# Performance work log

Hardware: AMD Instinct MI355X
Metric: run time of the kernel (lower is better)

The kernel has to match this reference:

```python
import jax, jax.numpy as jnp
import numpy as np

NUM_BLOCKS = 8
SPARSITY = 0.01
HARD_FRAC = 1.0
LN_EPS = 1e-5


def layer_norm(x, w, b):
    mu = jnp.mean(x, axis=-1, keepdims=True)
    var = jnp.mean(jnp.square(x - mu), axis=-1, keepdims=True)
    return (x - mu) * jax.lax.rsqrt(var + LN_EPS) * w + b


def softshrink(v, lam):
    return jnp.sign(v) * jnp.maximum(jnp.abs(v) - lam, 0.0)


def afno2d(x, w1, b1, w2, b2):
    # x: [B,H,W,C] float32
    bias = x
    B, H, W, C = x.shape
    nb = NUM_BLOCKS
    bs = C // nb
    xf = jnp.fft.rfft2(x, axes=(1, 2), norm='ortho')  # [B,H,W//2+1,C] complex
    Wf = W // 2 + 1
    xf = xf.reshape(B, H, Wf, nb, bs)
    total_modes = H // 2 + 1
    kept = int(total_modes * HARD_FRAC)
    lo = total_modes - kept
    hi = min(H, total_modes + kept)
    xs = xf[:, lo:hi, :kept]  # [B,hs,kept,nb,bs]
    xr, xi = xs.real, xs.imag
    o1r = jax.nn.relu(jnp.einsum('bhwki,kio->bhwko', xr, w1[0])
                      - jnp.einsum('bhwki,kio->bhwko', xi, w1[1]) + b1[0])
    o1i = jax.nn.relu(jnp.einsum('bhwki,kio->bhwko', xi, w1[0])
                      + jnp.einsum('bhwki,kio->bhwko', xr, w1[1]) + b1[1])
    o2r = (jnp.einsum('bhwko,koi->bhwki', o1r, w2[0])
           - jnp.einsum('bhwko,koi->bhwki', o1i, w2[1]) + b2[0])
    o2i = (jnp.einsum('bhwko,koi->bhwki', o1i, w2[0])
           + jnp.einsum('bhwko,koi->bhwki', o1r, w2[1]) + b2[1])
    o2r = softshrink(o2r, SPARSITY)
    o2i = softshrink(o2i, SPARSITY)
    oc = o2r + 1j * o2i
    full = jnp.zeros((B, H, Wf, nb, bs), dtype=oc.dtype)
    full = full.at[:, lo:hi, :kept].set(oc)
    full = full.reshape(B, H, Wf, C)
    out = jnp.fft.irfft2(full, s=(H, W), axes=(1, 2), norm='ortho')
    return out + bias


def setup_inputs() -> dict:
    key = jax.random.key(0)
    ks = jax.random.split(key, 12)
    B, H, W, C = 2, 90, 180, 768
    nb = NUM_BLOCKS
    bs = C // nb
    hidden = 4 * C
    scale = 0.02
    return {
        'x': jax.random.normal(ks[0], (B, H, W, C), jnp.float32),
        'norm1_w': jnp.ones((C,), jnp.float32),
        'norm1_b': jnp.zeros((C,), jnp.float32),
        'w1': scale * jax.random.normal(ks[1], (2, nb, bs, bs), jnp.float32),
        'b1': scale * jax.random.normal(ks[2], (2, nb, bs), jnp.float32),
        'w2': scale * jax.random.normal(ks[3], (2, nb, bs, bs), jnp.float32),
        'b2': scale * jax.random.normal(ks[4], (2, nb, bs), jnp.float32),
        'norm2_w': jnp.ones((C,), jnp.float32),
        'norm2_b': jnp.zeros((C,), jnp.float32),
        'fc1_w': jax.random.normal(ks[5], (C, hidden), jnp.float32) * (1.0 / np.sqrt(C)),
        'fc1_b': jnp.zeros((hidden,), jnp.float32),
        'fc2_w': jax.random.normal(ks[6], (hidden, C), jnp.float32) * (1.0 / np.sqrt(hidden)),
        'fc2_b': jnp.zeros((C,), jnp.float32),
    }


def reference(x, norm1_w, norm1_b, w1, b1, w2, b2, norm2_w, norm2_b,
              fc1_w, fc1_b, fc2_w, fc2_b):
    residual = x
    h = layer_norm(x, norm1_w, norm1_b)
    h = afno2d(h, w1, b1, w2, b2)
    # double_skip=True
    h = h + residual
    residual = h
    h = layer_norm(h, norm2_w, norm2_b)
    h = jax.nn.gelu(h @ fc1_w + fc1_b, approximate=False)
    h = h @ fc2_w + fc2_b
    return h + residual
```

## Files before the change

### kernel.cpp

```cpp
#include <hip/hip_runtime.h>
#include <hip/hip_bf16.h>

#define B_    2
#define H_    90
#define W_    180
#define C_    768
#define WFK   46
#define NBK   8
#define BSK   96
#define HID   3072
#define NTOK  (B_*H_*W_)
#define MPAD  32512
#define NPOS  (B_*H_*WFK)
#define LAM   0.01f

typedef __attribute__((ext_vector_type(8))) short short8;
typedef __attribute__((ext_vector_type(4))) float f32x4;

__device__ __forceinline__ float bf2f(short u) {
    union { unsigned int i; float f; } z;
    z.i = ((unsigned int)(unsigned short)u) << 16;
    return z.f;
}
__device__ __forceinline__ short f2b(float f) {
    return (short)__bfloat16_as_ushort(__float2bfloat16(f));
}

__device__ __forceinline__ void gload_lds16(const void* g, void* l) {
    __builtin_amdgcn_global_load_lds((const __attribute__((address_space(1))) void*)g,
                                     (__attribute__((address_space(3))) void*)l, 16, 0, 0);
}

__device__ __forceinline__ float gelu_f(float v) {
    float u = v * (0.7978845608028654f + 0.03567740813636141f * v * v);
    float au = fabsf(u);
    float e = __expf(2.f * au);
    float t = 1.f - 2.f / (e + 1.f);
    t = copysignf(t, u);
    return 0.5f * v * (1.f + t);
}

__global__ __launch_bounds__(256) void init_tables_kernel(__hip_bfloat16* Tw, __hip_bfloat16* Twf,
                                                          __hip_bfloat16* Thf, __hip_bfloat16* Thi) {
    int i = blockIdx.x * 256 + threadIdx.x;
    const float S = 0.00785674201318386f;
    if (i < 192 * 96) {
        int w = i / 96, k = i % 96;
        int j = k >> 1, odd = k & 1;
        float val = 0.f;
        if (w < W_ && j < WFK) {
            float th = (float)((w * j) % W_) * (float)(6.283185307179586476925286766559 / 180.0);
            if (odd) val = (j == 0) ? 0.f : -2.f * S * sinf(th);
            else     val = (j == 0) ? S : 2.f * S * cosf(th);
        }
        Tw[i] = __float2bfloat16(val);
    }
    if (i < 96 * 192) {
        int r = i / 192, w = i % 192;
        int wf = r >> 1, odd = r & 1;
        float val = 0.f;
        if (w < W_ && wf < WFK) {
            float th = (float)((w * wf) % W_) * (float)(6.283185307179586476925286766559 / 180.0);
            val = odd ? -S * sinf(th) : S * cosf(th);
        }
        Twf[i] = __float2bfloat16(val);
    }
    if (i < 192 * 192) {
        int r = i / 192, j = i % 192;
        float vf = 0.f, vi = 0.f;
        if (r < 180 && j < 180) {
            int k = r >> 1, ro = r & 1, h = j >> 1, jo = j & 1;
            float th = (float)((k * h) % H_) * (float)(6.283185307179586476925286766559 / 90.0);
            float c = cosf(th), s = sinf(th);
            vf = ro ? (jo ? c : -s) : (jo ? s : c);
            vi = ro ? (jo ? c : s) : (jo ? -s : c);
        }
        Thf[i] = __float2bfloat16(vf);
        Thi[i] = __float2bfloat16(vi);
    }
}

__global__ __launch_bounds__(256) void wprep_kernel(
        const float* __restrict__ w1, const float* __restrict__ b1,
        const float* __restrict__ w2, const float* __restrict__ b2,
        __hip_bfloat16* __restrict__ wbig, float* __restrict__ bbig)
{
    int idx = blockIdx.x * 256 + threadIdx.x;
    if (idx < 2 * NBK * 192 * 192) {
        int k = idx % 192;
        int o = (idx / 192) % 192;
        int nb = (idx / (192 * 192)) % NBK;
        int L = idx / (192 * 192 * NBK);
        const float* w = L ? w2 : w1;
        const float* wr = w + (size_t)nb * BSK * BSK;
        const float* wi = w + (size_t)(NBK + nb) * BSK * BSK;
        int kk = k % BSK, oo = o % BSK;
        float val;
        if (o < BSK)  val = (k < BSK) ? wr[kk * BSK + oo] : -wi[kk * BSK + oo];
        else          val = (k < BSK) ? wi[kk * BSK + oo] :  wr[kk * BSK + oo];
        wbig[((size_t)(L * NBK + nb) * 192 + o) * 192 + k] = __float2bfloat16(val);
    }
    if (idx < 2 * NBK * 192) {
        int o = idx % 192;
        int nb = (idx / 192) % NBK;
        int L = idx / (192 * NBK);
        const float* b = L ? b2 : b1;
        bbig[idx] = (o < BSK) ? b[nb * BSK + o] : b[(NBK + nb) * BSK + (o - BSK)];
    }
}

__global__ __launch_bounds__(256) void ln_kernel(const float* __restrict__ in,
        const float* __restrict__ w, const float* __restrict__ b,
        __hip_bfloat16* __restrict__ outb, int ntok_valid)
{
    int tok = blockIdx.x;
    int tid = threadIdx.x;
    size_t base = (size_t)tok * C_;
    if (tok >= ntok_valid) {
        __hip_bfloat16 z = __float2bfloat16(0.f);
        outb[base + tid] = z; outb[base + tid + 256] = z; outb[base + tid + 512] = z;
        return;
    }
    float x0 = in[base + tid], x1 = in[base + tid + 256], x2 = in[base + tid + 512];
    float s = x0 + x1 + x2;
    float q = x0*x0 + x1*x1 + x2*x2;
#pragma unroll
    for (int off = 32; off > 0; off >>= 1) { s += __shfl_down(s, off); q += __shfl_down(q, off); }
    __shared__ float rs[4], rq[4];
    int wid = tid >> 6, lane = tid & 63;
    if (lane == 0) { rs[wid] = s; rq[wid] = q; }
    __syncthreads();
    float ts = rs[0] + rs[1] + rs[2] + rs[3];
    float tq = rq[0] + rq[1] + rq[2] + rq[3];
    float mu = ts * (1.f / C_);
    float var = tq * (1.f / C_) - mu * mu;
    float rstd = rsqrtf(var + 1e-5f);
#pragma unroll
    for (int k = 0; k < 3; ++k) {
        int c = tid + k * 256;
        float xv = (k == 0 ? x0 : (k == 1 ? x1 : x2));
        outb[base + c] = __float2bfloat16((xv - mu) * rstd * w[c] + b[c]);
    }
}

__global__ __launch_bounds__(256) void wfft_kernel(const __hip_bfloat16* __restrict__ h1,
        short* __restrict__ f1r, short* __restrict__ f1i,
        const __hip_bfloat16* __restrict__ Twf)
{
    __shared__ __hip_bfloat16 Xt[64 * 200];
    int slab = blockIdx.x;
    int c0 = blockIdx.y * 64;
    int tid = threadIdx.x, wid = tid >> 6, lane = tid & 63;
    int lrow = lane & 15, lk8 = lane >> 4;
    const short* src = (const short*)h1 + (size_t)slab * W_ * C_ + c0;
    short* X = (short*)Xt;
    for (int i = tid; i < W_ * 8; i += 256) {
        int w = i >> 3, c8 = (i & 7) * 8;
        short8 v = *(const short8*)&src[(size_t)w * C_ + c8];
#pragma unroll
        for (int j = 0; j < 8; ++j) X[(c8 + j) * 200 + w] = v[j];
    }
    for (int z = tid; z < 64 * 12; z += 256) {
        int c = z / 12, w = 180 + z % 12;
        Xt[c * 200 + w] = __float2bfloat16(0.f);
    }
    __syncthreads();
    const short* Tp = (const short*)Twf;
    f32x4 zero = {0.f, 0.f, 0.f, 0.f};
    f32x4 acc[6];
#pragma unroll
    for (int m = 0; m < 6; ++m) acc[m] = zero;
#pragma unroll
    for (int ks = 0; ks < 6; ++ks) {
        short8 bf = *(const short8*)&X[(wid * 16 + lrow) * 200 + ks * 32 + lk8 * 8];
#pragma unroll
        for (int m = 0; m < 6; ++m) {
            short8 af = *(const short8*)&Tp[(m * 16 + lrow) * 192 + ks * 32 + lk8 * 8];
            acc[m] = __builtin_amdgcn_mfma_f32_16x16x32_bf16(af, bf, acc[m], 0, 0, 0);
        }
    }
    int crow = (lane >> 4) * 4, ccol = lane & 15;
#pragma unroll
    for (int m = 0; m < 6; ++m)
#pragma unroll
        for (int j = 0; j < 4; ++j) {
            int r = m * 16 + crow + j;
            int wf = r >> 1;
            if (wf >= WFK) continue;
            size_t o = ((size_t)slab * WFK + wf) * C_ + c0 + wid * 16 + ccol;
            if (r & 1) f1i[o] = f2b(acc[m][j]);
            else       f1r[o] = f2b(acc[m][j]);
        }
}

__global__ __launch_bounds__(256) void hdft_kernel(short* __restrict__ dr, short* __restrict__ di,
        const __hip_bfloat16* __restrict__ Th)
{
    __shared__ __hip_bfloat16 Xt[64 * 200];
    int bwf = blockIdx.x;
    int b = bwf / WFK, wf = bwf % WFK;
    int c0 = blockIdx.y * 64;
    int tid = threadIdx.x, wid = tid >> 6, lane = tid & 63;
    int lrow = lane & 15, lk8 = lane >> 4;
    size_t base = ((size_t)(b * H_) * WFK + wf) * C_ + c0;
    short* X = (short*)Xt;
    for (int i = tid; i < H_ * 8; i += 256) {
        int h = i >> 3, c8 = (i & 7) * 8;
        size_t a = base + (size_t)h * WFK * C_ + c8;
        short8 re = *(const short8*)&dr[a];
        short8 im = *(const short8*)&di[a];
#pragma unroll
        for (int j = 0; j < 8; ++j) {
            X[(c8 + j) * 200 + 2 * h]     = re[j];
            X[(c8 + j) * 200 + 2 * h + 1] = im[j];
        }
    }
    for (int z = tid; z < 64 * 12; z += 256) {
        int c = z / 12, j = 180 + z % 12;
        Xt[c * 200 + j] = __float2bfloat16(0.f);
    }
    __syncthreads();
    const short* Tp = (const short*)Th;
    f32x4 zero = {0.f, 0.f, 0.f, 0.f};
    f32x4 acc[3][4];
#pragma unroll
    for (int m = 0; m < 3; ++m)
#pragma unroll
        for (int n = 0; n < 4; ++n) acc[m][n] = zero;
#pragma unroll
    for (int ks = 0; ks < 6; ++ks) {
        short8 af[3], bf[4];
#pragma unroll
        for (int m = 0; m < 3; ++m)
            af[m] = *(const short8*)&Tp[(wid * 48 + m * 16 + lrow) * 192 + ks * 32 + lk8 * 8];
#pragma unroll
        for (int n = 0; n < 4; ++n)
            bf[n] = *(const short8*)&X[(n * 16 + lrow) * 200 + ks * 32 + lk8 * 8];
#pragma unroll
        for (int m = 0; m < 3; ++m)
#pragma unroll
            for (int n = 0; n < 4; ++n)
                acc[m][n] = __builtin_amdgcn_mfma_f32_16x16x32_bf16(af[m], bf[n], acc[m][n], 0, 0, 0);
    }
    int crow = (lane >> 4) * 4, ccol = lane & 15;
#pragma unroll
    for (int m = 0; m < 3; ++m)
#pragma unroll
        for (int j = 0; j < 4; ++j) {
            int r = wid * 48 + m * 16 + crow + j;
            int kh = r >> 1;
            if (kh >= H_) continue;
#pragma unroll
            for (int n = 0; n < 4; ++n) {
                size_t o = base + (size_t)kh * WFK * C_ + n * 16 + ccol;
                if (r & 1) di[o] = f2b(acc[m][n][j]);
                else       dr[o] = f2b(acc[m][n][j]);
            }
        }
}

__global__ __launch_bounds__(256) void blockmlp_mfma_kernel(
        short* __restrict__ vr, short* __restrict__ vi,
        const __hip_bfloat16* __restrict__ wbig, const float* __restrict__ bbig)
{
    __shared__ __hip_bfloat16 X1[64 * 200];
    __shared__ __hip_bfloat16 X2[64 * 200];
    int chunk = blockIdx.x;
    int nb = blockIdx.y;
    int tid = threadIdx.x, wid = tid >> 6, lane = tid & 63;
    int p0 = chunk * 64;
    short8 z8 = {0, 0, 0, 0, 0, 0, 0, 0};
    for (int i = tid; i < 64 * 24; i += 256) {
        int p = i / 24, q = i % 24;
        int pg = p0 + p;
        bool isr = q < 12;
        int c8 = (q % 12) * 8;
        short8 v = z8;
        if (pg < NPOS) {
            const short* src = isr ? vr : vi;
            v = *(const short8*)&src[(size_t)pg * C_ + nb * BSK + c8];
        }
        short* d = (short*)&X1[p * 200 + (isr ? 0 : 96) + c8];
#pragma unroll
        for (int j = 0; j < 8; ++j) d[j] = v[j];
    }
    __syncthreads();
    int n0 = wid * 48;
    int lrow = lane & 15, lk8 = lane >> 4;
    int crow = (lane >> 4) * 4, ccol = lane & 15;
    const short* W1 = (const short*)(wbig + (size_t)nb * 192 * 192);
    const short* W2 = (const short*)(wbig + (size_t)(NBK + nb) * 192 * 192);
    const float* bb1 = bbig + nb * 192;
    const float* bb2 = bbig + (NBK + nb) * 192;
    f32x4 zero = {0.f, 0.f, 0.f, 0.f};
    {
        f32x4 acc[4][3];
#pragma unroll
        for (int m = 0; m < 4; ++m)
#pragma unroll
            for (int n = 0; n < 3; ++n) acc[m][n] = zero;
#pragma unroll
        for (int k0 = 0; k0 < 192; k0 += 32) {
            short8 af[4], bf[3];
#pragma unroll
            for (int m = 0; m < 4; ++m)
                af[m] = *(const short8*)&X1[(m * 16 + lrow) * 200 + k0 + lk8 * 8];
#pragma unroll
            for (int n = 0; n < 3; ++n)
                bf[n] = *(const short8*)&W1[(size_t)(n0 + n * 16 + lrow) * 192 + k0 + lk8 * 8];
#pragma unroll
            for (int m = 0; m < 4; ++m)
#pragma unroll
                for (int n = 0; n < 3; ++n)
                    acc[m][n] = __builtin_amdgcn_mfma_f32_16x16x32_bf16(af[m], bf[n], acc[m][n], 0, 0, 0);
        }
        __syncthreads();
#pragma unroll
        for (int m = 0; m < 4; ++m)
#pragma unroll
            for (int j = 0; j < 4; ++j) {
                int row = m * 16 + crow + j;
#pragma unroll
                for (int n = 0; n < 3; ++n) {
                    int col = n0 + n * 16 + ccol;
                    float v = acc[m][n][j] + bb1[col];
                    X2[row * 200 + col] = __float2bfloat16(fmaxf(v, 0.f));
                }
            }
    }
    __syncthreads();
    {
        f32x4 acc[4][3];
#pragma unroll
        for (int m = 0; m < 4; ++m)
#pragma unroll
            for (int n = 0; n < 3; ++n) acc[m][n] = zero;
#pragma unroll
        for (int k0 = 0; k0 < 192; k0 += 32) {
            short8 af[4], bf[3];
#pragma unroll
            for (int m = 0; m < 4; ++m)
                af[m] = *(const short8*)&X2[(m * 16 + lrow) * 200 + k0 + lk8 * 8];
#pragma unroll
            for (int n = 0; n < 3; ++n)
                bf[n] = *(const short8*)&W2[(size_t)(n0 + n * 16 + lrow) * 192 + k0 + lk8 * 8];
#pragma unroll
            for (int m = 0; m < 4; ++m)
#pragma unroll
                for (int n = 0; n < 3; ++n)
                    acc[m][n] = __builtin_amdgcn_mfma_f32_16x16x32_bf16(af[m], bf[n], acc[m][n], 0, 0, 0);
        }
#pragma unroll
        for (int m = 0; m < 4; ++m)
#pragma unroll
            for (int j = 0; j < 4; ++j) {
                int row = m * 16 + crow + j;
                int pg = p0 + row;
                if (pg >= NPOS) continue;
#pragma unroll
                for (int n = 0; n < 3; ++n) {
                    int col = n0 + n * 16 + ccol;
                    float v = acc[m][n][j] + bb2[col];
                    v = v > LAM ? v - LAM : (v < -LAM ? v + LAM : 0.f);
                    if (col < BSK) vr[(size_t)pg * C_ + nb * BSK + col] = f2b(v);
                    else           vi[(size_t)pg * C_ + nb * BSK + col - BSK] = f2b(v);
                }
            }
    }
}

__global__ __launch_bounds__(256) void iwfft_kernel(
        const short* __restrict__ inr, const short* __restrict__ ini,
        const __hip_bfloat16* __restrict__ h1, const float* __restrict__ x,
        float* __restrict__ out, const __hip_bfloat16* __restrict__ Tw)
{
    __shared__ __hip_bfloat16 Yt[64 * 104];
    int slab = blockIdx.x;
    int c0 = blockIdx.y * 64;
    int tid = threadIdx.x, wid = tid >> 6, lane = tid & 63;
    int lrow = lane & 15, lk8 = lane >> 4;
    size_t sb = (size_t)slab * WFK * C_ + c0;
    short* Y = (short*)Yt;
    for (int i = tid; i < WFK * 8; i += 256) {
        int wf = i >> 3, c8 = (i & 7) * 8;
        size_t a = sb + (size_t)wf * C_ + c8;
        short8 re = *(const short8*)&inr[a];
        short8 im = *(const short8*)&ini[a];
#pragma unroll
        for (int j = 0; j < 8; ++j) {
            Y[(c8 + j) * 104 + 2 * wf]     = re[j];
            Y[(c8 + j) * 104 + 2 * wf + 1] = im[j];
        }
    }
    {
        int c = tid >> 2, kk = 92 + (tid & 3);
        Yt[c * 104 + kk] = __float2bfloat16(0.f);
    }
    __syncthreads();
    const short* Tp = (const short*)Tw;
    f32x4 zero = {0.f, 0.f, 0.f, 0.f};
    f32x4 acc[3][4];
#pragma unroll
    for (int m = 0; m < 3; ++m)
#pragma unroll
        for (int n = 0; n < 4; ++n) acc[m][n] = zero;
#pragma unroll
    for (int ks = 0; ks < 3; ++ks) {
        short8 af[3], bf[4];
#pragma unroll
        for (int m = 0; m < 3; ++m)
            af[m] = *(const short8*)&Tp[(wid * 48 + m * 16 + lrow) * 96 + ks * 32 + lk8 * 8];
#pragma unroll
        for (int n = 0; n < 4; ++n)
            bf[n] = *(const short8*)&Y[(n * 16 + lrow) * 104 + ks * 32 + lk8 * 8];
#pragma unroll
        for (int m = 0; m < 3; ++m)
#pragma unroll
            for (int n = 0; n < 4; ++n)
                acc[m][n] = __builtin_amdgcn_mfma_f32_16x16x32_bf16(af[m], bf[n], acc[m][n], 0, 0, 0);
    }
    int crow = (lane >> 4) * 4, ccol = lane & 15;
    const short* hp = (const short*)h1;
#pragma unroll
    for (int m = 0; m < 3; ++m)
#pragma unroll
        for (int j = 0; j < 4; ++j) {
            int w = wid * 48 + m * 16 + crow + j;
            if (w >= W_) continue;
            size_t o = ((size_t)slab * W_ + w) * C_ + c0;
#pragma unroll
            for (int n = 0; n < 4; ++n) {
                int col = n * 16 + ccol;
                out[o + col] = acc[m][n][j] + bf2f(hp[o + col]) + x[o + col];
            }
        }
}

__global__ __launch_bounds__(256) void transpose_cvt_kernel(const float* __restrict__ Wm,
        __hip_bfloat16* __restrict__ Wt, int R, int Ccol)
{
    __shared__ float tile[32][33];
    int c0 = blockIdx.x * 32, r0 = blockIdx.y * 32;
    int tid = threadIdx.x;
    int tc = tid & 31, tr = tid >> 5;
#pragma unroll
    for (int k = 0; k < 4; ++k)
        tile[tr + k * 8][tc] = Wm[(size_t)(r0 + tr + k * 8) * Ccol + c0 + tc];
    __syncthreads();
    int rr = tid & 31, cc = tid >> 5;
#pragma unroll
    for (int k = 0; k < 4; ++k)
        Wt[(size_t)(c0 + cc + k * 8) * R + r0 + rr] = __float2bfloat16(tile[rr][cc + k * 8]);
}

template<int EPI>
__global__ __launch_bounds__(512, 1) void gemm_kernel(
        const short* __restrict__ A, const short* __restrict__ Bt,
        const float* __restrict__ bias,
        __hip_bfloat16* __restrict__ obf, float* __restrict__ of32,
        const float* __restrict__ res, int N, int K, int mvalid, int MT, int NT)
{
    __shared__ short lds[73728];
    int nwg = MT * NT;
    int orig = blockIdx.x;
    int xcd = orig & 7, loc = orig >> 3;
    int q = nwg >> 3, rm = nwg & 7;
    int wg = (xcd < rm ? xcd * (q + 1) : rm * (q + 1) + (xcd - rm) * q) + loc;
    const int SUPER = 4;
    int per = SUPER * NT;
    int sidx = wg / per, offs = wg % per;
    int rows = MT - sidx * SUPER; if (rows > SUPER) rows = SUPER;
    int mt = sidx * SUPER + offs % rows;
    int nt = offs / rows;
    size_t m0 = (size_t)mt * 256, n0 = (size_t)nt * 128;

    int tid = threadIdx.x;
    int wid = tid >> 6, lane = tid & 63;
    int wmidx = wid >> 1, wnidx = wid & 1;
    int lrow = lane & 15, lk8 = lane >> 4;
    int rswz = (lk8 ^ ((lrow >> 1) & 3)) * 16;

    int sr = tid >> 2;
    int soct = (tid & 3) ^ ((sr >> 1) & 3);
    const short* Agbase = A + (m0 + sr) * (size_t)K + soct * 8;
    const short* Bgbase = Bt + (n0 + sr) * (size_t)K + soct * 8;
    int dA = sr * 64 + (tid & 3) * 16;
    f32x4 zero = {0.f, 0.f, 0.f, 0.f};
    f32x4 acc[4][4];
#pragma unroll
    for (int i = 0; i < 4; ++i)
#pragma unroll
        for (int j = 0; j < 4; ++j) acc[i][j] = zero;

    auto stage = [&](int buf, int kt) {
        const short* As0 = Agbase + kt * 64;
        const short* Bs0 = Bgbase + kt * 64;
        char* Ab = (char*)lds + buf * 49152 + dA;
        char* Bb = (char*)lds + buf * 49152 + 32768 + dA;
#pragma unroll
        for (int ksh = 0; ksh < 2; ++ksh) {
            gload_lds16(As0 + ksh * 32, Ab + ksh * 16384);
            gload_lds16(As0 + ksh * 32 + (size_t)128 * K, Ab + ksh * 16384 + 8192);
            gload_lds16(Bs0 + ksh * 32, Bb + ksh * 8192);
        }
    };

    int abase = (wmidx * 64 + lrow) * 64 + rswz;
    int bbase = 32768 + (wnidx * 64 + lrow) * 64 + rswz;

    int NK = K >> 6;
    stage(0, 0); stage(1, 1);
    for (int t = 0; t < NK; ++t) {
        int buf = t % 3;
        if (t + 2 < NK) stage((t + 2) % 3, t + 2);
        if (t + 2 < NK)      asm volatile("s_waitcnt vmcnt(12)" ::: "memory");
        else if (t + 1 < NK) asm volatile("s_waitcnt vmcnt(6)" ::: "memory");
        else                 asm volatile("s_waitcnt vmcnt(0)" ::: "memory");
        __builtin_amdgcn_sched_barrier(0);
        __builtin_amdgcn_s_barrier();
        __builtin_amdgcn_sched_barrier(0);
#pragma unroll
        for (int ks = 0; ks < 2; ++ks) {
            const char* L = (const char*)lds;
            short8 af[4], bfr[4];
            int ao = buf * 49152 + ks * 16384 + abase;
            int bo = buf * 49152 + ks * 8192 + bbase;
#pragma unroll
            for (int mf = 0; mf < 4; ++mf) af[mf] = *(const short8*)(L + ao + mf * 1024);
#pragma unroll
            for (int nf = 0; nf < 4; ++nf) bfr[nf] = *(const short8*)(L + bo + nf * 1024);
            asm volatile("s_waitcnt lgkmcnt(0)" ::: "memory");
            __builtin_amdgcn_sched_barrier(0);
            __builtin_amdgcn_s_setprio(1);
#pragma unroll
            for (int mf = 0; mf < 4; ++mf)
#pragma unroll
                for (int nf = 0; nf < 4; ++nf)
                    acc[mf][nf] = __builtin_amdgcn_mfma_f32_16x16x32_bf16(af[mf], bfr[nf], acc[mf][nf], 0, 0, 0);
            __builtin_amdgcn_s_setprio(0);
        }
        __builtin_amdgcn_sched_barrier(0);
        __builtin_amdgcn_s_barrier();
        __builtin_amdgcn_sched_barrier(0);
    }

    int crow = (lane >> 4) * 4;
    int ccol = lane & 15;
#pragma unroll
    for (int mf = 0; mf < 4; ++mf) {
#pragma unroll
        for (int j = 0; j < 4; ++j) {
            size_t r = m0 + wmidx * 64 + mf * 16 + crow + j;
            if (EPI == 1 && r >= (size_t)mvalid) continue;
#pragma unroll
            for (int nf = 0; nf < 4; ++nf) {
                size_t cidx = n0 + wnidx * 64 + nf * 16 + ccol;
                float v = acc[mf][nf][j] + bias[cidx];
                if (EPI == 0) {
                    obf[r * N + cidx] = __float2bfloat16(gelu_f(v));
                } else {
                    of32[r * N + cidx] = v + res[r * N + cidx];
                }
            }
        }
    }
}

extern "C" void kernel_launch(void* const* d_in, const int* in_sizes, int n_in,
                              void* d_out, int out_size, void* d_ws, size_t ws_size,
                              hipStream_t stream) {
    (void)in_sizes; (void)n_in; (void)out_size;
    const float* x    = (const float*)d_in[0];
    const float* n1w  = (const float*)d_in[1];
    const float* n1b  = (const float*)d_in[2];
    const float* w1   = (const float*)d_in[3];
    const float* b1   = (const float*)d_in[4];
    const float* w2   = (const float*)d_in[5];
    const float* b2   = (const float*)d_in[6];
    const float* n2w  = (const float*)d_in[7];
    const float* n2b  = (const float*)d_in[8];
    const float* fc1w = (const float*)d_in[9];
    const float* fc1b = (const float*)d_in[10];
    const float* fc2w = (const float*)d_in[11];
    const float* fc2b = (const float*)d_in[12];
    float* out = (float*)d_out;

    const size_t fl_region1 = (size_t)MPAD * C_ / 2;
    const size_t fl_f1      = (size_t)NPOS * C_;
    const size_t fl_tb1     = (size_t)MPAD * HID / 2;
    const size_t fl_tb2     = (size_t)64 * 256 * HID / 2;
    const size_t fl_wx      = 2712576 + 4096;
    const size_t need1 = (fl_region1 + fl_tb1 + fl_wx) * 4;
    const size_t need2 = (fl_region1 + ((fl_f1 > fl_tb2) ? fl_f1 : fl_tb2) + fl_wx) * 4;
    int nch = (ws_size >= need1) ? 1 : (ws_size >= need2) ? 2 : 4;
    size_t fl_tb = (nch == 1) ? fl_tb1 : (nch == 2) ? fl_tb2 : 0;
    size_t fl_big = (fl_f1 > fl_tb) ? fl_f1 : fl_tb;

    float* wsf = (float*)d_ws;
    size_t off = 0;
    auto alloc = [&](size_t nfloats) { float* p = wsf + off; off += (nfloats + 63) & ~(size_t)63; return p; };
    float* region1   = alloc(fl_region1);
    float* regionBig = alloc(fl_big);
    __hip_bfloat16* w1t = (__hip_bfloat16*)alloc((size_t)HID * C_ / 2);
    __hip_bfloat16* w2t = (__hip_bfloat16*)alloc((size_t)HID * C_ / 2);
    __hip_bfloat16* wbig = (__hip_bfloat16*)alloc((size_t)2 * NBK * 192 * 192 / 2);
    float* bbig = alloc(2 * NBK * 192);
    __hip_bfloat16* Tw  = (__hip_bfloat16*)alloc(192 * 96 / 2);
    __hip_bfloat16* Twf = (__hip_bfloat16*)alloc(96 * 192 / 2);
    __hip_bfloat16* Thf = (__hip_bfloat16*)alloc(192 * 192 / 2);
    __hip_bfloat16* Thi = (__hip_bfloat16*)alloc(192 * 192 / 2);

    __hip_bfloat16* h1b = (__hip_bfloat16*)region1;
    __hip_bfloat16* h3  = (__hip_bfloat16*)region1;
    short* f1r = (short*)regionBig;
    short* f1i = f1r + (size_t)NPOS * C_;
    __hip_bfloat16* tb  = (__hip_bfloat16*)regionBig;

    init_tables_kernel<<<144, 256, 0, stream>>>(Tw, Twf, Thf, Thi);
    wprep_kernel<<<(2 * NBK * 192 * 192 + 255) / 256, 256, 0, stream>>>(w1, b1, w2, b2, wbig, bbig);
    transpose_cvt_kernel<<<dim3(HID / 32, C_ / 32), 256, 0, stream>>>(fc1w, w1t, C_, HID);
    transpose_cvt_kernel<<<dim3(C_ / 32, HID / 32), 256, 0, stream>>>(fc2w, w2t, HID, C_);

    ln_kernel<<<NTOK, 256, 0, stream>>>(x, n1w, n1b, h1b, NTOK);
    wfft_kernel<<<dim3(B_ * H_, 12), 256, 0, stream>>>(h1b, f1r, f1i, Twf);
    hdft_kernel<<<dim3(B_ * WFK, 12), 256, 0, stream>>>(f1r, f1i, Thf);
    blockmlp_mfma_kernel<<<dim3(130, NBK), 256, 0, stream>>>(f1r, f1i, wbig, bbig);
    hdft_kernel<<<dim3(B_ * WFK, 12), 256, 0, stream>>>(f1r, f1i, Thi);
    iwfft_kernel<<<dim3(B_ * H_, 12), 256, 0, stream>>>(f1r, f1i, h1b, x, out, Tw);
    ln_kernel<<<MPAD, 256, 0, stream>>>(out, n2w, n2b, h3, NTOK);

    int tilesArr[4], ntiles = 0;
    if (nch == 1)      { tilesArr[0] = 127; ntiles = 1; }
    else if (nch == 2) { tilesArr[0] = 64; tilesArr[1] = 63; ntiles = 2; }
    else               { tilesArr[0] = 32; tilesArr[1] = 32; tilesArr[2] = 32; tilesArr[3] = 31; ntiles = 4; }
    int baseT = 0;
    for (int c = 0; c < ntiles; ++c) {
        int tiles = tilesArr[c];
        size_t baseRow = (size_t)baseT * 256;
        gemm_kernel<0><<<tiles * (HID / 128), 512, 0, stream>>>(
            (const short*)(h3 + baseRow * C_), (const short*)w1t, fc1b,
            tb, nullptr, nullptr, HID, C_, 0, tiles, HID / 128);
        gemm_kernel<1><<<tiles * (C_ / 128), 512, 0, stream>>>(
            (const short*)tb, (const short*)w2t, fc2b,
            nullptr, out + baseRow * C_, out + baseRow * C_, C_, HID, NTOK - (int)baseRow, tiles, C_ / 128);
        baseT += tiles;
    }
}
```

Measured before the change: 802.0 us.

## Split GEMM k-tile into two phases with finer-grained load/compute interleave

Restructures the triple-buffered MLP GEMM main loop so each 64-wide k-tile is handled as two 32-wide half-phases. Each phase issues half of the next stage's global-to-LDS loads right after reading its own fragments. It then waits on a finer vmcnt (9/6/3/0) instead of one wait per tile. This aims to spread memory issue across the MFMA work and overlap it better, at the cost of an extra barrier per half-tile and more delicate vmcnt bookkeeping.

```diff
diff --git a/kernel.cpp b/kernel.cpp
--- a/kernel.cpp
+++ b/kernel.cpp
@@ -492,56 +492,61 @@
 #pragma unroll
         for (int j = 0; j < 4; ++j) acc[i][j] = zero;
 
-    auto stage = [&](int buf, int kt) {
-        const short* As0 = Agbase + kt * 64;
-        const short* Bs0 = Bgbase + kt * 64;
-        char* Ab = (char*)lds + buf * 49152 + dA;
-        char* Bb = (char*)lds + buf * 49152 + 32768 + dA;
-#pragma unroll
-        for (int ksh = 0; ksh < 2; ++ksh) {
-            gload_lds16(As0 + ksh * 32, Ab + ksh * 16384);
-            gload_lds16(As0 + ksh * 32 + (size_t)128 * K, Ab + ksh * 16384 + 8192);
-            gload_lds16(Bs0 + ksh * 32, Bb + ksh * 8192);
-        }
+    auto stagepair = [&](int buf, int kt, int kh) {
+        const short* As = Agbase + kt * 64 + kh * 32;
+        char* Ad = (char*)lds + buf * 49152 + kh * 16384 + dA;
+        gload_lds16(As, Ad);
+        gload_lds16(As + (size_t)128 * K, Ad + 8192);
+        const short* Bs = Bgbase + kt * 64 + kh * 32;
+        char* Bd = (char*)lds + buf * 49152 + 32768 + kh * 8192 + dA;
+        gload_lds16(Bs, Bd);
     };
 
     int abase = (wmidx * 64 + lrow) * 64 + rswz;
     int bbase = 32768 + (wnidx * 64 + lrow) * 64 + rswz;
-
-    int NK = K >> 6;
-    stage(0, 0); stage(1, 1);
-    for (int t = 0; t < NK; ++t) {
-        int buf = t % 3;
-        if (t + 2 < NK) stage((t + 2) % 3, t + 2);
-        if (t + 2 < NK)      asm volatile("s_waitcnt vmcnt(12)" ::: "memory");
-        else if (t + 1 < NK) asm volatile("s_waitcnt vmcnt(6)" ::: "memory");
-        else                 asm volatile("s_waitcnt vmcnt(0)" ::: "memory");
+    auto phase = [&](int buf, int kh, int kt_stage, bool do_stage, int waitN) {
+        const char* L = (const char*)lds;
+        short8 af[4], bfr[4];
+        int ao = buf * 49152 + kh * 16384 + abase;
+        int bo = buf * 49152 + kh * 8192 + bbase;
+#pragma unroll
+        for (int mf = 0; mf < 4; ++mf) af[mf] = *(const short8*)(L + ao + mf * 1024);
+#pragma unroll
+        for (int nf = 0; nf < 4; ++nf) bfr[nf] = *(const short8*)(L + bo + nf * 1024);
+        if (do_stage) stagepair(kt_stage % 3, kt_stage, kh);
+        __builtin_amdgcn_sched_barrier(0);
+        __builtin_amdgcn_s_barrier();
+        asm volatile("s_waitcnt lgkmcnt(0)" ::: "memory");
+        __builtin_amdgcn_sched_barrier(0);
+        __builtin_amdgcn_s_setprio(1);
+#pragma unroll
+        for (int mf = 0; mf < 4; ++mf)
+#pragma unroll
+            for (int nf = 0; nf < 4; ++nf)
+                acc[mf][nf] = __builtin_amdgcn_mfma_f32_16x16x32_bf16(af[mf], bfr[nf], acc[mf][nf], 0, 0, 0);
+        __builtin_amdgcn_s_setprio(0);
+        if (waitN == 9)      asm volatile("s_waitcnt vmcnt(9)" ::: "memory");
+        else if (waitN == 6) asm volatile("s_waitcnt vmcnt(6)" ::: "memory");
+        else if (waitN == 3) asm volatile("s_waitcnt vmcnt(3)" ::: "memory");
+        else if (waitN == 0) asm volatile("s_waitcnt vmcnt(0)" ::: "memory");
         __builtin_amdgcn_sched_barrier(0);
         __builtin_amdgcn_s_barrier();
         __builtin_amdgcn_sched_barrier(0);
-#pragma unroll
-        for (int ks = 0; ks < 2; ++ks) {
-            const char* L = (const char*)lds;
-            short8 af[4], bfr[4];
-            int ao = buf * 49152 + ks * 16384 + abase;
-            int bo = buf * 49152 + ks * 8192 + bbase;
-#pragma unroll
-            for (int mf = 0; mf < 4; ++mf) af[mf] = *(const short8*)(L + ao + mf * 1024);
-#pragma unroll
-            for (int nf = 0; nf < 4; ++nf) bfr[nf] = *(const short8*)(L + bo + nf * 1024);
-            asm volatile("s_waitcnt lgkmcnt(0)" ::: "memory");
-            __builtin_amdgcn_sched_barrier(0);
-            __builtin_amdgcn_s_setprio(1);
-#pragma unroll
-            for (int mf = 0; mf < 4; ++mf)
-#pragma unroll
-                for (int nf = 0; nf < 4; ++nf)
-                    acc[mf][nf] = __builtin_amdgcn_mfma_f32_16x16x32_bf16(af[mf], bfr[nf], acc[mf][nf], 0, 0, 0);
-            __builtin_amdgcn_s_setprio(0);
-        }
-        __builtin_amdgcn_sched_barrier(0);
-        __builtin_amdgcn_s_barrier();
-        __builtin_amdgcn_sched_barrier(0);
+    };
+
+    int NK = K >> 6;
+    stagepair(0, 0, 0); stagepair(0, 0, 1);
+    stagepair(1, 1, 0); stagepair(1, 1, 1);
+    asm volatile("s_waitcnt vmcnt(9)" ::: "memory");
+    __builtin_amdgcn_sched_barrier(0);
+    __builtin_amdgcn_s_barrier();
+    for (int t = 0; t < NK; ++t) {
+        int buf = t % 3;
+        bool st = (t + 2 < NK);
+        int w0 = st ? 9 : (t == NK - 2 ? 6 : 0);
+        int w1 = st ? 9 : (t == NK - 2 ? 3 : -1);
+        phase(buf, 0, t + 2, st, w0);
+        phase(buf, 1, t + 2, st, w1);
     }
 
     int crow = (lane >> 4) * 4;
```

Measured after the change: 753.8 us. 1.06x faster.

## Enlarge GEMM tiles to 256x256 with double-buffered LDS pipeline

Applied to the files above, without the earlier changes.

The MLP GEMM kernel now uses 256x256 output tiles with 8 waves arranged 2x4, each computing 128x64. The LDS layout changes to 128-byte rows with an XOR swizzle over eight 16-byte chunks. The triple-buffered prefetch-two-ahead pipeline becomes double buffering: each iteration waits for all loads, then issues the next stage after the barrier. The larger tile raises data reuse per load and halves the number of workgroups. In exchange it doubles accumulator registers and weakens latency hiding, since the kernel waits on vmcnt(0) every iteration.

```diff
diff --git a/kernel.cpp b/kernel.cpp
--- a/kernel.cpp
+++ b/kernel.cpp
@@ -460,7 +460,7 @@
         __hip_bfloat16* __restrict__ obf, float* __restrict__ of32,
         const float* __restrict__ res, int N, int K, int mvalid, int MT, int NT)
 {
-    __shared__ short lds[73728];
+    __shared__ short lds[65536];
     int nwg = MT * NT;
     int orig = blockIdx.x;
     int xcd = orig & 7, loc = orig >> 3;
@@ -472,89 +472,89 @@
     int rows = MT - sidx * SUPER; if (rows > SUPER) rows = SUPER;
     int mt = sidx * SUPER + offs % rows;
     int nt = offs / rows;
-    size_t m0 = (size_t)mt * 256, n0 = (size_t)nt * 128;
+    size_t m0 = (size_t)mt * 256, n0 = (size_t)nt * 256;
 
     int tid = threadIdx.x;
     int wid = tid >> 6, lane = tid & 63;
-    int wmidx = wid >> 1, wnidx = wid & 1;
-    int lrow = lane & 15, lk8 = lane >> 4;
-    int rswz = (lk8 ^ ((lrow >> 1) & 3)) * 16;
-
-    int sr = tid >> 2;
-    int soct = (tid & 3) ^ ((sr >> 1) & 3);
-    const short* Agbase = A + (m0 + sr) * (size_t)K + soct * 8;
-    const short* Bgbase = Bt + (n0 + sr) * (size_t)K + soct * 8;
-    int dA = sr * 64 + (tid & 3) * 16;
+    int wm = wid >> 2, wn = wid & 3;
+    int lrow = lane & 15, lk8 = lane >> 4, l7 = lrow & 7;
+
+    int srow = tid >> 3;
+    int sobase = tid & 7;
     f32x4 zero = {0.f, 0.f, 0.f, 0.f};
-    f32x4 acc[4][4];
-#pragma unroll
-    for (int i = 0; i < 4; ++i)
+    f32x4 acc[8][4];
+#pragma unroll
+    for (int i = 0; i < 8; ++i)
 #pragma unroll
         for (int j = 0; j < 4; ++j) acc[i][j] = zero;
 
     auto stage = [&](int buf, int kt) {
-        const short* As0 = Agbase + kt * 64;
-        const short* Bs0 = Bgbase + kt * 64;
-        char* Ab = (char*)lds + buf * 49152 + dA;
-        char* Bb = (char*)lds + buf * 49152 + 32768 + dA;
-#pragma unroll
-        for (int ksh = 0; ksh < 2; ++ksh) {
-            gload_lds16(As0 + ksh * 32, Ab + ksh * 16384);
-            gload_lds16(As0 + ksh * 32 + (size_t)128 * K, Ab + ksh * 16384 + 8192);
-            gload_lds16(Bs0 + ksh * 32, Bb + ksh * 8192);
+        char* Ld = (char*)lds + buf * 65536 + (size_t)tid * 16;
+#pragma unroll
+        for (int p = 0; p < 4; ++p) {
+            int row = p * 64 + srow;
+            int soct = sobase ^ (row & 7);
+            gload_lds16(A + (m0 + row) * (size_t)K + kt * 64 + soct * 8, Ld + p * 8192);
+            gload_lds16(Bt + (n0 + row) * (size_t)K + kt * 64 + soct * 8, Ld + 32768 + p * 8192);
         }
     };
 
-    int abase = (wmidx * 64 + lrow) * 64 + rswz;
-    int bbase = 32768 + (wnidx * 64 + lrow) * 64 + rswz;
+    int aoff0 = (wm * 128 + lrow) * 128 + ((lk8) ^ l7) * 16;
+    int aoff1 = (wm * 128 + lrow) * 128 + ((4 + lk8) ^ l7) * 16;
+    int boff0 = 32768 + (wn * 64 + lrow) * 128 + ((lk8) ^ l7) * 16;
+    int boff1 = 32768 + (wn * 64 + lrow) * 128 + ((4 + lk8) ^ l7) * 16;
 
     int NK = K >> 6;
-    stage(0, 0); stage(1, 1);
+    stage(0, 0);
     for (int t = 0; t < NK; ++t) {
-        int buf = t % 3;
-        if (t + 2 < NK) stage((t + 2) % 3, t + 2);
-        if (t + 2 < NK)      asm volatile("s_waitcnt vmcnt(12)" ::: "memory");
-        else if (t + 1 < NK) asm volatile("s_waitcnt vmcnt(6)" ::: "memory");
-        else                 asm volatile("s_waitcnt vmcnt(0)" ::: "memory");
+        int buf = t & 1;
+        asm volatile("s_waitcnt vmcnt(0)" ::: "memory");
         __builtin_amdgcn_sched_barrier(0);
         __builtin_amdgcn_s_barrier();
         __builtin_amdgcn_sched_barrier(0);
-#pragma unroll
-        for (int ks = 0; ks < 2; ++ks) {
-            const char* L = (const char*)lds;
-            short8 af[4], bfr[4];
-            int ao = buf * 49152 + ks * 16384 + abase;
-            int bo = buf * 49152 + ks * 8192 + bbase;
-#pragma unroll
-            for (int mf = 0; mf < 4; ++mf) af[mf] = *(const short8*)(L + ao + mf * 1024);
-#pragma unroll
-            for (int nf = 0; nf < 4; ++nf) bfr[nf] = *(const short8*)(L + bo + nf * 1024);
+        if (t + 1 < NK) stage(buf ^ 1, t + 1);
+        const char* L = (const char*)lds + buf * 65536;
+        short8 bfr[4][2];
+#pragma unroll
+        for (int nf = 0; nf < 4; ++nf) {
+            bfr[nf][0] = *(const short8*)(L + boff0 + nf * 2048);
+            bfr[nf][1] = *(const short8*)(L + boff1 + nf * 2048);
+        }
+#pragma unroll
+        for (int p = 0; p < 4; ++p) {
+            short8 af[2][2];
+#pragma unroll
+            for (int mh = 0; mh < 2; ++mh) {
+                af[mh][0] = *(const short8*)(L + aoff0 + (2 * p + mh) * 2048);
+                af[mh][1] = *(const short8*)(L + aoff1 + (2 * p + mh) * 2048);
+            }
             asm volatile("s_waitcnt lgkmcnt(0)" ::: "memory");
             __builtin_amdgcn_sched_barrier(0);
             __builtin_amdgcn_s_setprio(1);
 #pragma unroll
-            for (int mf = 0; mf < 4; ++mf)
-#pragma unroll
-                for (int nf = 0; nf < 4; ++nf)
-                    acc[mf][nf] = __builtin_amdgcn_mfma_f32_16x16x32_bf16(af[mf], bfr[nf], acc[mf][nf], 0, 0, 0);
+            for (int mh = 0; mh < 2; ++mh)
+#pragma unroll
+                for (int nf = 0; nf < 4; ++nf) {
+                    acc[2 * p + mh][nf] = __builtin_amdgcn_mfma_f32_16x16x32_bf16(
+                        af[mh][0], bfr[nf][0], acc[2 * p + mh][nf], 0, 0, 0);
+                    acc[2 * p + mh][nf] = __builtin_amdgcn_mfma_f32_16x16x32_bf16(
+                        af[mh][1], bfr[nf][1], acc[2 * p + mh][nf], 0, 0, 0);
+                }
             __builtin_amdgcn_s_setprio(0);
         }
-        __builtin_amdgcn_sched_barrier(0);
-        __builtin_amdgcn_s_barrier();
-        __builtin_amdgcn_sched_barrier(0);
     }
 
     int crow = (lane >> 4) * 4;
     int ccol = lane & 15;
 #pragma unroll
-    for (int mf = 0; mf < 4; ++mf) {
+    for (int mf = 0; mf < 8; ++mf) {
 #pragma unroll
         for (int j = 0; j < 4; ++j) {
-            size_t r = m0 + wmidx * 64 + mf * 16 + crow + j;
+            size_t r = m0 + wm * 128 + mf * 16 + crow + j;
             if (EPI == 1 && r >= (size_t)mvalid) continue;
 #pragma unroll
             for (int nf = 0; nf < 4; ++nf) {
-                size_t cidx = n0 + wnidx * 64 + nf * 16 + ccol;
+                size_t cidx = n0 + wn * 64 + nf * 16 + ccol;
                 float v = acc[mf][nf][j] + bias[cidx];
                 if (EPI == 0) {
                     obf[r * N + cidx] = __float2bfloat16(gelu_f(v));
@@ -637,12 +637,12 @@
     for (int c = 0; c < ntiles; ++c) {
         int tiles = tilesArr[c];
         size_t baseRow = (size_t)baseT * 256;
-        gemm_kernel<0><<<tiles * (HID / 128), 512, 0, stream>>>(
+        gemm_kernel<0><<<tiles * (HID / 256), 512, 0, stream>>>(
             (const short*)(h3 + baseRow * C_), (const short*)w1t, fc1b,
-            tb, nullptr, nullptr, HID, C_, 0, tiles, HID / 128);
-        gemm_kernel<1><<<tiles * (C_ / 128), 512, 0, stream>>>(
+            tb, nullptr, nullptr, HID, C_, 0, tiles, HID / 256);
+        gemm_kernel<1><<<tiles * (C_ / 256), 512, 0, stream>>>(
             (const short*)tb, (const short*)w2t, fc2b,
-            nullptr, out + baseRow * C_, out + baseRow * C_, C_, HID, NTOK - (int)baseRow, tiles, C_ / 128);
+            nullptr, out + baseRow * C_, out + baseRow * C_, C_, HID, NTOK - (int)baseRow, tiles, C_ / 256);
         baseT += tiles;
     }
 }
```

Measured after the change: 705.8 us. 12.0% less time.
